# Kernel optimization log

Measured on AMD Instinct MI355X. Metric: run time of the kernel, lower is better.

## Reference

```python
import jax, jax.numpy as jnp
import numpy as np

N, E, D_IN, D_H = 50000, 800000, 128, 128


def setup_inputs() -> dict:
    key = jax.random.key(0)
    ks = jax.random.split(key, 8)
    x = jax.random.normal(ks[0], (N, D_IN), dtype=jnp.float32)
    edge_index = jax.random.randint(ks[1], (2, E), 0, N, dtype=jnp.int64)
    edge_attr = jax.random.normal(ks[2], (E, D_H), dtype=jnp.float32)
    s_in = 1.0 / np.sqrt(D_IN)
    W_mean = jax.random.uniform(ks[3], (D_H, D_IN), jnp.float32, -s_in, s_in)
    b_mean = jax.random.uniform(ks[4], (D_H,), jnp.float32, -s_in, s_in)
    W_std = jax.random.uniform(ks[5], (D_H, D_IN), jnp.float32, -s_in, s_in)
    b_std = jax.random.uniform(ks[6], (D_H,), jnp.float32, -s_in, s_in)
    return {"x": x, "edge_index": edge_index, "edge_attr": edge_attr,
            "W_mean": W_mean, "b_mean": b_mean, "W_std": W_std, "b_std": b_std}


def _gcn(x, edge_index, edge_attr, W, b):
    # linear projection: [N, D_H]
    h = x @ W.T + b
    row, col = edge_index[0], edge_index[1]
    n = x.shape[0]
    # degree of target nodes (col), symmetric-ish normalization
    deg = jax.ops.segment_sum(jnp.ones(row.shape[0], dtype=h.dtype), col, num_segments=n)
    deg_inv_sqrt = jnp.where(deg > 0, jax.lax.rsqrt(jnp.maximum(deg, 1.0)) * jnp.where(deg > 0, 1.0, 0.0), 0.0)
    norm = deg_inv_sqrt[row] * deg_inv_sqrt[col]  # [E]
    msg = norm[:, None] * (h[row] + edge_attr)     # [E, D_H]
    out = jax.ops.segment_sum(msg, col, num_segments=n) + h  # aggregate at target + residual
    return out


def reference(x, edge_index, edge_attr, W_mean, b_mean, W_std, b_std):
    mean = _gcn(x, edge_index, edge_attr, W_mean, b_mean)
    std = _gcn(x, edge_index, edge_attr, W_std, b_std)
    return (mean, std)
```

## Files before the change

kernel.cpp:

```cpp
#include <hip/hip_runtime.h>
#include <math.h>

#define N_NODES 50000
#define N_EDGES 800000
#define D 128

#define TILE_R 32
#define HIST_BLKS ((N_EDGES + 255) / 256)
#define SCAT_BLKS HIST_BLKS
#define GEMM_BLKS ((N_NODES + TILE_R - 1) / TILE_R)

typedef float        vf2 __attribute__((ext_vector_type(2)));
typedef unsigned int vu2 __attribute__((ext_vector_type(2)));

static __device__ __forceinline__ unsigned f2bf(float f) {
    unsigned u = __float_as_uint(f);
    u += 0x7FFFu + ((u >> 16) & 1u);
    return u >> 16;
}

__global__ __launch_bounds__(256) void hist_kernel(const int* __restrict__ ei,
                                                   int* __restrict__ count) {
    int e = blockIdx.x * blockDim.x + threadIdx.x;
    if (e < N_EDGES) {
        atomicAdd(&count[ei[N_EDGES + e]], 1);
    }
}

__global__ __launch_bounds__(1024) void scan1_kernel(const int* __restrict__ count,
                                                     int* __restrict__ offset,
                                                     float* __restrict__ dis,
                                                     int* __restrict__ bsum) {
    __shared__ int wsum[16];
    const int tid = threadIdx.x;
    const int lane = tid & 63;
    const int wid = tid >> 6;
    const int i = blockIdx.x * 1024 + tid;

    int c = (i < N_NODES) ? count[i] : 0;
    int inc = c;
#pragma unroll
    for (int d = 1; d < 64; d <<= 1) {
        int v = __shfl_up(inc, d, 64);
        if (lane >= d) inc += v;
    }
    if (lane == 63) wsum[wid] = inc;
    __syncthreads();
    if (wid == 0) {
        int s = (lane < 16) ? wsum[lane] : 0;
#pragma unroll
        for (int d = 1; d < 16; d <<= 1) {
            int v = __shfl_up(s, d, 64);
            if (lane >= d) s += v;
        }
        if (lane < 16) wsum[lane] = s;
    }
    __syncthreads();
    int wpre = (wid > 0) ? wsum[wid - 1] : 0;
    if (i < N_NODES) {
        offset[i] = wpre + inc - c;
        dis[i] = (c > 0) ? rsqrtf((float)c) : 0.0f;
    }
    if (tid == 0) bsum[blockIdx.x] = wsum[15];
}

__global__ __launch_bounds__(1024) void fixup_kernel(const int* __restrict__ bsum,
                                                     int* __restrict__ offset,
                                                     int* __restrict__ cur) {
    __shared__ int pre_s;
    const int tid = threadIdx.x;
    const int blk = blockIdx.x;
    if ((tid >> 6) == 0) {
        int lane = tid & 63;
        int s = 0;
        for (int j = lane; j < blk; j += 64) s += bsum[j];
#pragma unroll
        for (int d = 32; d > 0; d >>= 1) s += __shfl_xor(s, d, 64);
        if (lane == 0) pre_s = s;
    }
    __syncthreads();
    int i = blk * 1024 + tid;
    if (i < N_NODES) {
        int o = offset[i] + pre_s;
        offset[i] = o;
        cur[i] = o;
    }
}

__global__ __launch_bounds__(256) void fused_kernel(
    const float* __restrict__ x,
    const float* __restrict__ Wm, const float* __restrict__ bm,
    const float* __restrict__ Ws, const float* __restrict__ bs,
    unsigned* __restrict__ hpk,
    const int* __restrict__ ei, const float* __restrict__ dis,
    int* __restrict__ cur, vu2* __restrict__ meta)
{
    __shared__ float xs[TILE_R][D];
    const int tid = threadIdx.x;

    if (blockIdx.x >= GEMM_BLKS) {
        int e = (blockIdx.x - GEMM_BLKS) * 256 + tid;
        if (e < N_EDGES) {
            int row = ei[e];
            int col = ei[N_EDGES + e];
            int p = atomicAdd(&cur[col], 1);
            vu2 v;
            v[0] = (unsigned)e;
            v[1] = (unsigned)row | (f2bf(dis[row]) << 16);
            meta[p] = v;
        }
        return;
    }

    const int r0 = blockIdx.x * TILE_R;

    for (int i = tid; i < TILE_R * D / 4; i += 256) {
        int rr = i / (D / 4);
        int cc = (i % (D / 4)) * 4;
        int r = r0 + rr;
        float4 v = make_float4(0.f, 0.f, 0.f, 0.f);
        if (r < N_NODES) v = *(const float4*)(x + (size_t)r * D + cc);
        *(float4*)(&xs[rr][cc]) = v;
    }
    __syncthreads();

    const int m = tid >> 7;
    const int p = (tid >> 1) & 63;
    const int rh = tid & 1;
    const int c0 = p * 2;
    const float* __restrict__ W = m ? Ws : Wm;
    const float* __restrict__ b = m ? bs : bm;
    const float b0 = b[c0], b1 = b[c0 + 1];

    float acc0[16], acc1[16];
#pragma unroll
    for (int rr = 0; rr < 16; ++rr) { acc0[rr] = b0; acc1[rr] = b1; }

    const float* __restrict__ Wr0 = W + (size_t)c0 * D;
    const float* __restrict__ Wr1 = W + (size_t)(c0 + 1) * D;

    for (int kc = 0; kc < D; kc += 32) {
        float w0[32], w1[32];
#pragma unroll
        for (int j = 0; j < 32; j += 4) {
            float4 a = *(const float4*)(Wr0 + kc + j);
            float4 bb = *(const float4*)(Wr1 + kc + j);
            w0[j] = a.x; w0[j+1] = a.y; w0[j+2] = a.z; w0[j+3] = a.w;
            w1[j] = bb.x; w1[j+1] = bb.y; w1[j+2] = bb.z; w1[j+3] = bb.w;
        }
#pragma unroll
        for (int rr = 0; rr < 16; ++rr) {
            const float* xr = &xs[rh * 16 + rr][kc];
#pragma unroll
            for (int j = 0; j < 32; j += 4) {
                float4 xv = *(const float4*)(xr + j);
                acc0[rr] = fmaf(xv.x, w0[j],     acc0[rr]);
                acc0[rr] = fmaf(xv.y, w0[j + 1], acc0[rr]);
                acc0[rr] = fmaf(xv.z, w0[j + 2], acc0[rr]);
                acc0[rr] = fmaf(xv.w, w0[j + 3], acc0[rr]);
                acc1[rr] = fmaf(xv.x, w1[j],     acc1[rr]);
                acc1[rr] = fmaf(xv.y, w1[j + 1], acc1[rr]);
                acc1[rr] = fmaf(xv.z, w1[j + 2], acc1[rr]);
                acc1[rr] = fmaf(xv.w, w1[j + 3], acc1[rr]);
            }
        }
    }

#pragma unroll
    for (int rr = 0; rr < 16; ++rr) {
        int r = r0 + rh * 16 + rr;
        if (r < N_NODES) {
            unsigned word = f2bf(acc0[rr]) | (f2bf(acc1[rr]) << 16);
            hpk[(size_t)r * 128 + p * 2 + m] = word;
        }
    }
}

__global__ __launch_bounds__(256) void agg_kernel(
    const float* __restrict__ eap, const vu2* __restrict__ hpk,
    const vu2* __restrict__ meta,
    const int* __restrict__ offset, const int* __restrict__ cur,
    const float* __restrict__ dis,
    float* __restrict__ om, float* __restrict__ os)
{
    const int tid = threadIdx.x;
    const int lane = tid & 63;
    const int wid = tid >> 6;
    const int n = blockIdx.x * 4 + wid;

    const int start = offset[n];
    const int end = cur[n];
    const float dc = dis[n];
    const int k = lane * 2;

    vu2 hpn = hpk[(size_t)n * 64 + lane];

    float amx = 0.f, amy = 0.f, asx = 0.f, asy = 0.f;

    for (int jb = start; jb < end; jb += 64) {
        vu2 mt = (vu2)(0);
        if (jb + lane < end)
            mt = __builtin_nontemporal_load(meta + jb + lane);
        const int mm = min(64, end - jb);

        for (int j0 = 0; j0 < mm; j0 += 8) {
            vf2 eav[8]; vu2 hpv[8]; float drv[8];
#pragma unroll
            for (int u = 0; u < 8; ++u) {
                const int jx = j0 + u;
                const int jj = (jx < mm) ? jx : (mm - 1);
                unsigned ev = (unsigned)__builtin_amdgcn_readlane((int)mt[0], jj);
                unsigned pk = (unsigned)__builtin_amdgcn_readlane((int)mt[1], jj);
                eav[u] = __builtin_nontemporal_load(
                    (const vf2*)(eap + (size_t)ev * D + k));
                hpv[u] = hpk[(size_t)(pk & 0xFFFFu) * 64 + lane];
                drv[u] = (jx < mm) ? __uint_as_float(pk & 0xFFFF0000u) : 0.0f;
            }
#pragma unroll
            for (int u = 0; u < 8; ++u) {
                float h0 = __uint_as_float(hpv[u][0] << 16);
                float h1 = __uint_as_float(hpv[u][0] & 0xFFFF0000u);
                float g0 = __uint_as_float(hpv[u][1] << 16);
                float g1 = __uint_as_float(hpv[u][1] & 0xFFFF0000u);
                amx = fmaf(drv[u], h0 + eav[u][0], amx);
                amy = fmaf(drv[u], h1 + eav[u][1], amy);
                asx = fmaf(drv[u], g0 + eav[u][0], asx);
                asy = fmaf(drv[u], g1 + eav[u][1], asy);
            }
        }
    }

    const size_t ob = (size_t)n * D + k;
    vf2 o0, o1;
    o0[0] = __uint_as_float(hpn[0] << 16)         + dc * amx;
    o0[1] = __uint_as_float(hpn[0] & 0xFFFF0000u) + dc * amy;
    o1[0] = __uint_as_float(hpn[1] << 16)         + dc * asx;
    o1[1] = __uint_as_float(hpn[1] & 0xFFFF0000u) + dc * asy;
    __builtin_nontemporal_store(o0, (vf2*)(om + ob));
    __builtin_nontemporal_store(o1, (vf2*)(os + ob));
}

extern "C" void kernel_launch(void* const* d_in, const int* in_sizes, int n_in,
                              void* d_out, int out_size, void* d_ws, size_t ws_size,
                              hipStream_t stream) {
    const float* x   = (const float*)d_in[0];
    const int*   ei  = (const int*)d_in[1];
    const float* ea  = (const float*)d_in[2];
    const float* Wm  = (const float*)d_in[3];
    const float* bm  = (const float*)d_in[4];
    const float* Ws  = (const float*)d_in[5];
    const float* bs  = (const float*)d_in[6];
    float* out = (float*)d_out;

    char* w = (char*)d_ws;
    int*   count  = (int*)w;     w += (size_t)N_NODES * 4;
    int*   offset = (int*)w;     w += (size_t)N_NODES * 4;
    int*   cur    = (int*)w;     w += (size_t)N_NODES * 4;
    float* dis    = (float*)w;   w += (size_t)N_NODES * 4;
    int*   bsum   = (int*)w;     w += 4096;
    vu2*   meta   = (vu2*)w;     w += (size_t)N_EDGES * 8;
    unsigned* hpk = (unsigned*)w;
    float* om = out;
    float* os = out + (size_t)N_NODES * D;

    const int SCAN_BLKS = (N_NODES + 1023) / 1024;

    hipMemsetAsync(count, 0, N_NODES * sizeof(int), stream);

    hist_kernel<<<HIST_BLKS, 256, 0, stream>>>(ei, count);

    scan1_kernel<<<SCAN_BLKS, 1024, 0, stream>>>(count, offset, dis, bsum);
    fixup_kernel<<<SCAN_BLKS, 1024, 0, stream>>>(bsum, offset, cur);

    fused_kernel<<<GEMM_BLKS + SCAT_BLKS, 256, 0, stream>>>(
        x, Wm, bm, Ws, bs, hpk, ei, dis, cur, meta);

    agg_kernel<<<N_NODES / 4, 256, 0, stream>>>(
        ea, (const vu2*)hpk, meta, offset, cur, dis, om, os);
}
```

Baseline: 262.6 us.

## Pre-permute edge_attr into CSR order as bf16 during scatter pass

The scatter phase now processes one edge per wavefront. It reads that edge's 128-float attribute row, packs it to bf16, and writes it into a CSR-ordered buffer at the atomically reserved slot. The aggregation kernel then streams edge attributes contiguously at half the bytes instead of gathering random fp32 rows. Per-edge meta shrinks to a single word. The cost is an extra full read of edge_attr plus a bf16 write in the fused kernel, and bf16 rounding of the edge attributes.

```diff
diff --git a/kernel.cpp b/kernel.cpp
--- a/kernel.cpp
+++ b/kernel.cpp
@@ -7,7 +7,7 @@
 
 #define TILE_R 32
 #define HIST_BLKS ((N_EDGES + 255) / 256)
-#define SCAT_BLKS HIST_BLKS
+#define SCAT_BLKS 8192
 #define GEMM_BLKS ((N_NODES + TILE_R - 1) / TILE_R)
 
 typedef float        vf2 __attribute__((ext_vector_type(2)));
@@ -92,22 +92,29 @@
     const float* __restrict__ Wm, const float* __restrict__ bm,
     const float* __restrict__ Ws, const float* __restrict__ bs,
     unsigned* __restrict__ hpk,
-    const int* __restrict__ ei, const float* __restrict__ dis,
-    int* __restrict__ cur, vu2* __restrict__ meta)
+    const int* __restrict__ ei, const float* __restrict__ ea,
+    const float* __restrict__ dis,
+    int* __restrict__ cur, unsigned* __restrict__ meta,
+    unsigned* __restrict__ eapk)
 {
     __shared__ float xs[TILE_R][D];
     const int tid = threadIdx.x;
 
     if (blockIdx.x >= GEMM_BLKS) {
-        int e = (blockIdx.x - GEMM_BLKS) * 256 + tid;
-        if (e < N_EDGES) {
+        const int lane = tid & 63;
+        const int gw = (blockIdx.x - GEMM_BLKS) * 4 + (tid >> 6);
+        const int nw = SCAT_BLKS * 4;
+        for (int e = gw; e < N_EDGES; e += nw) {
             int row = ei[e];
             int col = ei[N_EDGES + e];
-            int p = atomicAdd(&cur[col], 1);
-            vu2 v;
-            v[0] = (unsigned)e;
-            v[1] = (unsigned)row | (f2bf(dis[row]) << 16);
-            meta[p] = v;
+            vf2 v = __builtin_nontemporal_load((const vf2*)(ea + (size_t)e * D + 2 * lane));
+            unsigned pk = f2bf(v[0]) | (f2bf(v[1]) << 16);
+            int p = 0;
+            if (lane == 0) p = atomicAdd(&cur[col], 1);
+            p = __shfl(p, 0);
+            __builtin_nontemporal_store(pk, eapk + (size_t)p * 64 + lane);
+            if (lane == 0)
+                meta[p] = (unsigned)row | (f2bf(dis[row]) << 16);
         }
         return;
     }
@@ -177,8 +184,8 @@
 }
 
 __global__ __launch_bounds__(256) void agg_kernel(
-    const float* __restrict__ eap, const vu2* __restrict__ hpk,
-    const vu2* __restrict__ meta,
+    const unsigned* __restrict__ eapk, const vu2* __restrict__ hpk,
+    const unsigned* __restrict__ meta,
     const int* __restrict__ offset, const int* __restrict__ cur,
     const float* __restrict__ dis,
     float* __restrict__ om, float* __restrict__ os)
@@ -191,46 +198,46 @@
     const int start = offset[n];
     const int end = cur[n];
     const float dc = dis[n];
-    const int k = lane * 2;
 
     vu2 hpn = hpk[(size_t)n * 64 + lane];
 
     float amx = 0.f, amy = 0.f, asx = 0.f, asy = 0.f;
 
     for (int jb = start; jb < end; jb += 64) {
-        vu2 mt = (vu2)(0);
+        unsigned mt = 0;
         if (jb + lane < end)
             mt = __builtin_nontemporal_load(meta + jb + lane);
         const int mm = min(64, end - jb);
 
         for (int j0 = 0; j0 < mm; j0 += 8) {
-            vf2 eav[8]; vu2 hpv[8]; float drv[8];
+            unsigned eav[8]; vu2 hpv[8]; float drv[8];
 #pragma unroll
             for (int u = 0; u < 8; ++u) {
                 const int jx = j0 + u;
                 const int jj = (jx < mm) ? jx : (mm - 1);
-                unsigned ev = (unsigned)__builtin_amdgcn_readlane((int)mt[0], jj);
-                unsigned pk = (unsigned)__builtin_amdgcn_readlane((int)mt[1], jj);
+                unsigned pk = (unsigned)__builtin_amdgcn_readlane((int)mt, jj);
+                hpv[u] = hpk[(size_t)(pk & 0xFFFFu) * 64 + lane];
                 eav[u] = __builtin_nontemporal_load(
-                    (const vf2*)(eap + (size_t)ev * D + k));
-                hpv[u] = hpk[(size_t)(pk & 0xFFFFu) * 64 + lane];
+                    eapk + (size_t)(jb + jj) * 64 + lane);
                 drv[u] = (jx < mm) ? __uint_as_float(pk & 0xFFFF0000u) : 0.0f;
             }
 #pragma unroll
             for (int u = 0; u < 8; ++u) {
+                float eax = __uint_as_float(eav[u] << 16);
+                float eay = __uint_as_float(eav[u] & 0xFFFF0000u);
                 float h0 = __uint_as_float(hpv[u][0] << 16);
                 float h1 = __uint_as_float(hpv[u][0] & 0xFFFF0000u);
                 float g0 = __uint_as_float(hpv[u][1] << 16);
                 float g1 = __uint_as_float(hpv[u][1] & 0xFFFF0000u);
-                amx = fmaf(drv[u], h0 + eav[u][0], amx);
-                amy = fmaf(drv[u], h1 + eav[u][1], amy);
-                asx = fmaf(drv[u], g0 + eav[u][0], asx);
-                asy = fmaf(drv[u], g1 + eav[u][1], asy);
+                amx = fmaf(drv[u], h0 + eax, amx);
+                amy = fmaf(drv[u], h1 + eay, amy);
+                asx = fmaf(drv[u], g0 + eax, asx);
+                asy = fmaf(drv[u], g1 + eay, asy);
             }
         }
     }
 
-    const size_t ob = (size_t)n * D + k;
+    const size_t ob = (size_t)n * D + 2 * lane;
     vf2 o0, o1;
     o0[0] = __uint_as_float(hpn[0] << 16)         + dc * amx;
     o0[1] = __uint_as_float(hpn[0] & 0xFFFF0000u) + dc * amy;
@@ -253,13 +260,14 @@
     float* out = (float*)d_out;
 
     char* w = (char*)d_ws;
-    int*   count  = (int*)w;     w += (size_t)N_NODES * 4;
-    int*   offset = (int*)w;     w += (size_t)N_NODES * 4;
-    int*   cur    = (int*)w;     w += (size_t)N_NODES * 4;
-    float* dis    = (float*)w;   w += (size_t)N_NODES * 4;
-    int*   bsum   = (int*)w;     w += 4096;
-    vu2*   meta   = (vu2*)w;     w += (size_t)N_EDGES * 8;
-    unsigned* hpk = (unsigned*)w;
+    int*   count  = (int*)w;      w += (size_t)N_NODES * 4;
+    int*   offset = (int*)w;      w += (size_t)N_NODES * 4;
+    int*   cur    = (int*)w;      w += (size_t)N_NODES * 4;
+    float* dis    = (float*)w;    w += (size_t)N_NODES * 4;
+    int*   bsum   = (int*)w;      w += 4096;
+    unsigned* meta = (unsigned*)w; w += (size_t)N_EDGES * 4;
+    unsigned* hpk  = (unsigned*)w; w += (size_t)N_NODES * 128 * 4;
+    unsigned* eapk = (unsigned*)w;
     float* om = out;
     float* os = out + (size_t)N_NODES * D;
 
@@ -273,8 +281,8 @@
     fixup_kernel<<<SCAN_BLKS, 1024, 0, stream>>>(bsum, offset, cur);
 
     fused_kernel<<<GEMM_BLKS + SCAT_BLKS, 256, 0, stream>>>(
-        x, Wm, bm, Ws, bs, hpk, ei, dis, cur, meta);
+        x, Wm, bm, Ws, bs, hpk, ei, ea, dis, cur, meta, eapk);
 
     agg_kernel<<<N_NODES / 4, 256, 0, stream>>>(
-        ea, (const vu2*)hpk, meta, offset, cur, dis, om, os);
-}
+        eapk, (const vu2*)hpk, meta, offset, cur, dis, om, os);
+}
```

Result: slower. 703.2 us (+167.8%).
